# Kernel tuning notes

Measured on AMD Instinct MI355X. Metric: run time of the kernel, lower is better.

The kernel has to match this reference:

```python
import jax, jax.numpy as jnp
import numpy as np

B, T, C = 2, 2048, 768
H = 12
HD = C // H  # 64
DFF = 4 * C
EPS = 1e-5


def setup_inputs() -> dict:
    key = jax.random.key(0)
    ks = jax.random.split(key, 12)
    s = 0.02
    return {
        "x": jax.random.normal(ks[0], (B, T, C), dtype=jnp.float32),
        "ln1_g": jnp.ones((C,), jnp.float32),
        "ln1_b": jnp.zeros((C,), jnp.float32),
        "w_qkv": jax.random.normal(ks[1], (C, 3 * C), dtype=jnp.float32) * s,
        "w_o": jax.random.normal(ks[2], (C, C), dtype=jnp.float32) * s,
        "ln2_g": jnp.ones((C,), jnp.float32),
        "ln2_b": jnp.zeros((C,), jnp.float32),
        "w_fc": jax.random.normal(ks[3], (C, DFF), dtype=jnp.float32) * s,
        "b_fc": jnp.zeros((DFF,), jnp.float32),
        "w_proj": jax.random.normal(ks[4], (DFF, C), dtype=jnp.float32) * s,
        "b_proj": jnp.zeros((C,), jnp.float32),
    }


def _layernorm(x, g, b):
    mu = jnp.mean(x, axis=-1, keepdims=True)
    var = jnp.mean(jnp.square(x - mu), axis=-1, keepdims=True)
    return (x - mu) * jax.lax.rsqrt(var + EPS) * g + b


def _attn(x, w_qkv, w_o):
    b, t, c = x.shape
    qkv = x @ w_qkv  # [b,t,3c]
    q, k, v = jnp.split(qkv, 3, axis=-1)
    q = q.reshape(b, t, H, HD).transpose(0, 2, 1, 3)  # [b,h,t,d]
    k = k.reshape(b, t, H, HD).transpose(0, 2, 1, 3)
    v = v.reshape(b, t, H, HD).transpose(0, 2, 1, 3)
    att = jnp.einsum("bhqd,bhkd->bhqk", q, k) / jnp.sqrt(jnp.float32(HD))
    causal = jnp.tril(jnp.ones((t, t), dtype=bool))
    att = jnp.where(causal, att, -jnp.inf)
    att = jax.nn.softmax(att, axis=-1)
    y = jnp.einsum("bhqk,bhkd->bhqd", att, v)
    y = y.transpose(0, 2, 1, 3).reshape(b, t, c)
    return y @ w_o


def reference(x, ln1_g, ln1_b, w_qkv, w_o, ln2_g, ln2_b, w_fc, b_fc, w_proj, b_proj):
    x = x + _attn(_layernorm(x, ln1_g, ln1_b), w_qkv, w_o)
    h = _layernorm(x, ln2_g, ln2_b)
    h = jax.nn.gelu(h @ w_fc + b_fc, approximate=False)  # torch F.gelu default = exact erf
    x = x + (h @ w_proj + b_proj)
    return x
```

## Files before the change

### kernel.cpp

```cpp
#include <hip/hip_runtime.h>
#include <hip/hip_bf16.h>
#include <math.h>

#define T_SEQ 2048
#define NB 2
#define C_DIM 768
#define NH 12

typedef unsigned short ushort_t;
typedef __attribute__((ext_vector_type(8))) short short8;
typedef __attribute__((ext_vector_type(8))) unsigned short ushort8;
typedef __attribute__((ext_vector_type(4))) unsigned short ushortx4;
typedef __attribute__((ext_vector_type(4))) float floatx4;
typedef __attribute__((ext_vector_type(4))) _Float16 half4;

__device__ inline float bf2f(ushort_t u) {
    unsigned int x = ((unsigned int)u) << 16;
    return __uint_as_float(x);
}
__device__ inline ushort_t f2bf(float f) {
    unsigned int u = __float_as_uint(f);
    unsigned int r = (u + 0x7fffu + ((u >> 16) & 1u)) >> 16;
    return (ushort_t)r;
}
__device__ inline ushort_t f2h_bits(float f) {
    union { _Float16 h; ushort_t u; } cv;
    cv.h = (_Float16)f;
    return cv.u;
}

#if defined(__has_builtin)
#if __has_builtin(__builtin_amdgcn_global_load_lds)
#define HAVE_GLL 1
#endif
#endif

__device__ inline void gload_lds16(const ushort_t* g, ushort_t* l) {
#ifdef HAVE_GLL
    __builtin_amdgcn_global_load_lds(
        (const __attribute__((address_space(1))) void*)g,
        (__attribute__((address_space(3))) void*)l, 16, 0, 0);
#else
    int lane = threadIdx.x & 63;
    *(ushort8*)(l + lane * 8) = *(const ushort8*)g;
#endif
}

__global__ __launch_bounds__(256) void ln_kernel(const float* __restrict__ x,
                                                 const float* __restrict__ g,
                                                 const float* __restrict__ b,
                                                 ushort_t* __restrict__ out) {
    int row = blockIdx.x;
    int tid = threadIdx.x;
    int lane = tid & 63, wave = tid >> 6;
    const float* xr = x + (size_t)row * C_DIM;
    float v0 = xr[tid];
    float v1 = xr[tid + 256];
    float v2 = xr[tid + 512];
    float s = v0 + v1 + v2;
#pragma unroll
    for (int m = 32; m > 0; m >>= 1) s += __shfl_xor(s, m, 64);
    __shared__ float red[8];
    if (lane == 0) red[wave] = s;
    __syncthreads();
    float mean = (red[0] + red[1] + red[2] + red[3]) * (1.0f / C_DIM);
    float d0 = v0 - mean, d1 = v1 - mean, d2 = v2 - mean;
    float q = d0 * d0 + d1 * d1 + d2 * d2;
#pragma unroll
    for (int m = 32; m > 0; m >>= 1) q += __shfl_xor(q, m, 64);
    if (lane == 0) red[wave + 4] = q;
    __syncthreads();
    float var = (red[4] + red[5] + red[6] + red[7]) * (1.0f / C_DIM);
    float rstd = rsqrtf(var + 1e-5f);
    ushort_t* orow = out + (size_t)row * C_DIM;
    orow[tid]       = f2bf(d0 * rstd * g[tid]       + b[tid]);
    orow[tid + 256] = f2bf(d1 * rstd * g[tid + 256] + b[tid + 256]);
    orow[tid + 512] = f2bf(d2 * rstd * g[tid + 512] + b[tid + 512]);
}

__global__ __launch_bounds__(192) void combine_ln_kernel(const float* __restrict__ x,
                                                         const ushort_t* __restrict__ P,
                                                         const float* __restrict__ g,
                                                         const float* __restrict__ bb,
                                                         float* __restrict__ x2,
                                                         ushort_t* __restrict__ xn) {
    int row = blockIdx.x;
    int tid = threadIdx.x;
    int lane = tid & 63, wave = tid >> 6;
    int col = tid * 4;
    size_t idx = (size_t)row * C_DIM + col;
    floatx4 xv = *(const floatx4*)&x[idx];
    ushortx4 a = *(const ushortx4*)&P[idx];
    ushortx4 b2 = *(const ushortx4*)&P[3145728 + idx];
    ushortx4 c2 = *(const ushortx4*)&P[6291456 + idx];
    floatx4 v;
#pragma unroll
    for (int j = 0; j < 4; j++) v[j] = xv[j] + bf2f(a[j]) + bf2f(b2[j]) + bf2f(c2[j]);
    *(floatx4*)&x2[idx] = v;

    float s = v[0] + v[1] + v[2] + v[3];
#pragma unroll
    for (int m = 32; m > 0; m >>= 1) s += __shfl_xor(s, m, 64);
    __shared__ float red[6];
    if (lane == 0) red[wave] = s;
    __syncthreads();
    float mean = (red[0] + red[1] + red[2]) * (1.0f / C_DIM);
    floatx4 d;
#pragma unroll
    for (int j = 0; j < 4; j++) d[j] = v[j] - mean;
    float q = d[0] * d[0] + d[1] * d[1] + d[2] * d[2] + d[3] * d[3];
#pragma unroll
    for (int m = 32; m > 0; m >>= 1) q += __shfl_xor(q, m, 64);
    if (lane == 0) red[wave + 3] = q;
    __syncthreads();
    float var = (red[3] + red[4] + red[5]) * (1.0f / C_DIM);
    float rstd = rsqrtf(var + 1e-5f);
    floatx4 gv = *(const floatx4*)&g[col];
    floatx4 bv = *(const floatx4*)&bb[col];
    ushortx4 o;
#pragma unroll
    for (int j = 0; j < 4; j++) o[j] = f2bf(d[j] * rstd * gv[j] + bv[j]);
    *(ushortx4*)&xn[idx] = o;
}

__global__ __launch_bounds__(256) void wconv_kernel(const float* __restrict__ W,
                                                    ushort_t* __restrict__ WT,
                                                    int K, int N) {
    __shared__ ushort_t Tls[64 * 72];
    int tid = threadIdx.x;
    int k0 = blockIdx.x * 64, n0 = blockIdx.y * 64;
    int nl = (tid & 15) * 4;
    int kl = tid >> 4;
#pragma unroll
    for (int rr = 0; rr < 4; rr++) {
        int k = kl + rr * 16;
        floatx4 v = *(const floatx4*)&W[(size_t)(k0 + k) * N + n0 + nl];
#pragma unroll
        for (int j = 0; j < 4; j++) Tls[(nl + j) * 72 + k] = f2bf(v[j]);
    }
    __syncthreads();
    int no = tid >> 3;
    int ko = (tid & 7) * 8;
#pragma unroll
    for (int rr = 0; rr < 2; rr++) {
        int n = no + rr * 32;
        ushort8 t = *(const ushort8*)&Tls[n * 72 + ko];
        *(ushort8*)&WT[(size_t)(n0 + n) * K + k0 + ko] = t;
    }
}

__global__ __launch_bounds__(256) void kvprep_kernel(const ushort_t* __restrict__ qkv,
                                                     ushort_t* __restrict__ kh,
                                                     ushort_t* __restrict__ vtb) {
    __shared__ ushort_t Tls[64 * 18];
    int tid = threadIdx.x;
    int tb = blockIdx.x, h = blockIdx.y, b = blockIdx.z;
    const ushort_t* src = qkv + (size_t)b * T_SEQ * 2304;
    size_t hb = (size_t)(b * NH + h) * (T_SEQ * 64);

#pragma unroll
    for (int i = 0; i < 4; i++) {
        int idx = tid + i * 256;
        int t = tb * 16 + (idx >> 6), d = idx & 63;
        kh[hb + (size_t)t * 64 + d] = src[(size_t)t * 2304 + 768 + h * 64 + d];
    }
#pragma unroll
    for (int i = 0; i < 4; i++) {
        int idx = tid + i * 256;
        int t = idx >> 6, d = idx & 63;
        Tls[d * 18 + t] = f2h_bits(bf2f(src[(size_t)(tb * 16 + t) * 2304 + 1536 + h * 64 + d]));
    }
    __syncthreads();
    ushort_t* dst = vtb + hb + (size_t)tb * 1024;
#pragma unroll
    for (int i = 0; i < 4; i++) {
        int j = tid + i * 256;
        dst[j] = Tls[(j >> 4) * 18 + (j & 15)];
    }
}

template <int EPI>
__global__ __launch_bounds__(256) void gemm_bt_kernel(const ushort_t* __restrict__ A,
                                                      const ushort_t* __restrict__ BT,
                                                      const float* __restrict__ bias,
                                                      ushort_t* __restrict__ Cout,
                                                      int M, int N, int K) {
    __shared__ ushort_t As[128 * 64];
    __shared__ ushort_t Bs[128 * 64];
    int tid = threadIdx.x;
    int lane = tid & 63, wave = tid >> 6;
    int lane15 = lane & 15, quad = lane >> 4;
    int wr = wave >> 1, wc = wave & 1;
    int row0 = blockIdx.x * 128, col0 = blockIdx.y * 128;

    int srow = lane >> 3;
    int sseg = (lane & 7) ^ srow;
    const ushort_t* ag[4];
    const ushort_t* bg[4];
    ushort_t* la[4];
    ushort_t* lb[4];
#pragma unroll
    for (int j = 0; j < 4; j++) {
        int r = wave * 32 + j * 8;
        ag[j] = A + (size_t)(row0 + r + srow) * K + sseg * 8;
        bg[j] = BT + (size_t)(col0 + r + srow) * K + sseg * 8;
        la[j] = &As[r * 64];
        lb[j] = &Bs[r * 64];
    }

    floatx4 acc[4][4];
    floatx4 zero = {0.f, 0.f, 0.f, 0.f};
#pragma unroll
    for (int mt = 0; mt < 4; mt++)
#pragma unroll
        for (int nt = 0; nt < 4; nt++) acc[mt][nt] = zero;

    for (int k0 = 0; k0 < K; k0 += 64) {
#pragma unroll
        for (int j = 0; j < 4; j++) gload_lds16(ag[j] + k0, la[j]);
#pragma unroll
        for (int j = 0; j < 4; j++) gload_lds16(bg[j] + k0, lb[j]);
        __syncthreads();
#pragma unroll
        for (int ko = 0; ko < 2; ko++) {
            int slot = (quad + ko * 4) ^ (lane15 & 7);
            short8 af[4], bfm[4];
#pragma unroll
            for (int mt = 0; mt < 4; mt++)
                af[mt] = *(const short8*)&As[(wr * 64 + mt * 16 + lane15) * 64 + slot * 8];
#pragma unroll
            for (int nt = 0; nt < 4; nt++)
                bfm[nt] = *(const short8*)&Bs[(wc * 64 + nt * 16 + lane15) * 64 + slot * 8];
#pragma unroll
            for (int mt = 0; mt < 4; mt++)
#pragma unroll
                for (int nt = 0; nt < 4; nt++)
                    acc[mt][nt] = __builtin_amdgcn_mfma_f32_16x16x32_bf16(af[mt], bfm[nt], acc[mt][nt], 0, 0, 0);
        }
        __syncthreads();
    }

#pragma unroll
    for (int mt = 0; mt < 4; mt++) {
        int r_base = row0 + wr * 64 + mt * 16 + quad * 4;
#pragma unroll
        for (int nt = 0; nt < 4; nt++) {
            int cc = col0 + wc * 64 + nt * 16 + lane15;
            float bvv = (EPI == 2) ? bias[cc] : 0.f;
#pragma unroll
            for (int r = 0; r < 4; r++) {
                int rr = r_base + r;
                float v = acc[mt][nt][r] + bvv;
                if (EPI == 2) v = 0.5f * v * (1.f + erff(v * 0.70710678118f));
                Cout[(size_t)rr * N + cc] = f2bf(v);
            }
        }
    }
}

__global__ __launch_bounds__(256) void gemm_bt_split_kernel(const ushort_t* __restrict__ A,
                                                            const ushort_t* __restrict__ BT,
                                                            ushort_t* __restrict__ P,
                                                            int M, int N, int K, int klen) {
    __shared__ ushort_t As[128 * 64];
    __shared__ ushort_t Bs[128 * 64];
    int tid = threadIdx.x;
    int lane = tid & 63, wave = tid >> 6;
    int lane15 = lane & 15, quad = lane >> 4;
    int wr = wave >> 1, wc = wave & 1;
    int row0 = blockIdx.x * 128, col0 = blockIdx.y * 128;
    int kz = blockIdx.z * klen;

    int srow = lane >> 3;
    int sseg = (lane & 7) ^ srow;
    const ushort_t* ag[4];
    const ushort_t* bg[4];
    ushort_t* la[4];
    ushort_t* lb[4];
#pragma unroll
    for (int j = 0; j < 4; j++) {
        int r = wave * 32 + j * 8;
        ag[j] = A + (size_t)(row0 + r + srow) * K + kz + sseg * 8;
        bg[j] = BT + (size_t)(col0 + r + srow) * K + kz + sseg * 8;
        la[j] = &As[r * 64];
        lb[j] = &Bs[r * 64];
    }

    floatx4 acc[4][4];
    floatx4 zero = {0.f, 0.f, 0.f, 0.f};
#pragma unroll
    for (int mt = 0; mt < 4; mt++)
#pragma unroll
        for (int nt = 0; nt < 4; nt++) acc[mt][nt] = zero;

    for (int k0 = 0; k0 < klen; k0 += 64) {
#pragma unroll
        for (int j = 0; j < 4; j++) gload_lds16(ag[j] + k0, la[j]);
#pragma unroll
        for (int j = 0; j < 4; j++) gload_lds16(bg[j] + k0, lb[j]);
        __syncthreads();
#pragma unroll
        for (int ko = 0; ko < 2; ko++) {
            int slot = (quad + ko * 4) ^ (lane15 & 7);
            short8 af[4], bfm[4];
#pragma unroll
            for (int mt = 0; mt < 4; mt++)
                af[mt] = *(const short8*)&As[(wr * 64 + mt * 16 + lane15) * 64 + slot * 8];
#pragma unroll
            for (int nt = 0; nt < 4; nt++)
                bfm[nt] = *(const short8*)&Bs[(wc * 64 + nt * 16 + lane15) * 64 + slot * 8];
#pragma unroll
            for (int mt = 0; mt < 4; mt++)
#pragma unroll
                for (int nt = 0; nt < 4; nt++)
                    acc[mt][nt] = __builtin_amdgcn_mfma_f32_16x16x32_bf16(af[mt], bfm[nt], acc[mt][nt], 0, 0, 0);
        }
        __syncthreads();
    }

    ushort_t* Pz = P + (size_t)blockIdx.z * M * N;
#pragma unroll
    for (int mt = 0; mt < 4; mt++) {
        int r_base = row0 + wr * 64 + mt * 16 + quad * 4;
#pragma unroll
        for (int nt = 0; nt < 4; nt++) {
            int cc = col0 + wc * 64 + nt * 16 + lane15;
#pragma unroll
            for (int r = 0; r < 4; r++)
                Pz[(size_t)(r_base + r) * N + cc] = f2bf(acc[mt][nt][r]);
        }
    }
}

__global__ __launch_bounds__(256) void combine_bias_res_kernel(float* __restrict__ x2,
                                                               const float* __restrict__ bias,
                                                               const ushort_t* __restrict__ P) {
    int i = blockIdx.x * 256 + threadIdx.x;
    int col = (i * 4) % C_DIM;
    floatx4 xv = *(const floatx4*)&x2[i * 4];
    floatx4 bv = *(const floatx4*)&bias[col];
    ushortx4 a = *(const ushortx4*)&P[i * 4];
    ushortx4 b = *(const ushortx4*)&P[3145728 + i * 4];
    floatx4 o;
#pragma unroll
    for (int j = 0; j < 4; j++) o[j] = xv[j] + bv[j] + bf2f(a[j]) + bf2f(b[j]);
    *(floatx4*)&x2[i * 4] = o;
}

#define QSCALE 0.18033688f
__global__ __launch_bounds__(256) void attn_kernel(const ushort_t* __restrict__ qkv,
                                                   const ushort_t* __restrict__ kh,
                                                   const _Float16* __restrict__ vtb,
                                                   ushort_t* __restrict__ y) {
    __shared__ ushort_t Kb[2][4096];
    __shared__ ushort_t Vb[2][4096];
    int tid = threadIdx.x;
    int lane = tid & 63, wave = tid >> 6;
    int lane15 = lane & 15, quad = lane >> 4;
    int qt = 31 - (int)blockIdx.x;
    int q0 = qt * 64;
    int h = blockIdx.y, b = blockIdx.z;
    const ushort_t* base = qkv + (size_t)b * T_SEQ * 2304;
    size_t hb = (size_t)(b * NH + h) * (T_SEQ * 64);
    const ushort_t* khb = kh + hb;
    const ushort_t* vtbb = (const ushort_t*)(vtb + hb);

    int q = q0 + wave * 16 + lane15;
    int qmax_wave = q0 + wave * 16 + 15;
    short8 qf[2];
#pragma unroll
    for (int c = 0; c < 2; c++) {
        ushort8 qv = *(const ushort8*)(base + (size_t)q * 2304 + h * 64 + c * 32 + quad * 8);
        short8 qs;
#pragma unroll
        for (int j = 0; j < 8; j++) qs[j] = (short)f2bf(bf2f(qv[j]) * QSCALE);
        qf[c] = qs;
    }

    floatx4 o[4];
    floatx4 zero = {0.f, 0.f, 0.f, 0.f};
#pragma unroll
    for (int nt = 0; nt < 4; nt++) o[nt] = zero;
    float m_i = -1e30f, l_i = 0.f;

    int tiles = qt + 1;

    {
        int kb = 0;
        if (wave < 2) {
#pragma unroll
            for (int j = 0; j < 4; j++) {
                int r = wave * 4 + j;
                int i = r * 64 + lane;
                int key = i >> 3;
                int seg = ((i & 7) - (key & 7) + 8) & 7;
                gload_lds16(khb + (size_t)(kb + key) * 64 + seg * 8, &Kb[0][(size_t)r * 512]);
            }
        } else {
#pragma unroll
            for (int j = 0; j < 4; j++) {
                int r = (wave - 2) * 4 + j;
                gload_lds16(vtbb + (size_t)(kb >> 4) * 1024 + (size_t)r * 512 + lane * 8,
                            &Vb[0][(size_t)r * 512]);
            }
        }
    }

    for (int t = 0; t < tiles; t++) {
        int kb = t * 64;
        int cur = t & 1;
        __syncthreads();
        if (t + 1 < tiles) {
            int kb2 = kb + 64;
            int nxt = cur ^ 1;
            if (wave < 2) {
#pragma unroll
                for (int j = 0; j < 4; j++) {
                    int r = wave * 4 + j;
                    int i = r * 64 + lane;
                    int key = i >> 3;
                    int seg = ((i & 7) - (key & 7) + 8) & 7;
                    gload_lds16(khb + (size_t)(kb2 + key) * 64 + seg * 8, &Kb[nxt][(size_t)r * 512]);
                }
            } else {
#pragma unroll
                for (int j = 0; j < 4; j++) {
                    int r = (wave - 2) * 4 + j;
                    gload_lds16(vtbb + (size_t)(kb2 >> 4) * 1024 + (size_t)r * 512 + lane * 8,
                                &Vb[nxt][(size_t)r * 512]);
                }
            }
        }

        if (kb <= qmax_wave) {
            const ushort_t* Kc = Kb[cur];
            const _Float16* Vc = (const _Float16*)Vb[cur];

            floatx4 s[4];
#pragma unroll
            for (int sb = 0; sb < 4; sb++) {
                int key = sb * 16 + lane15;
                int s0i = key * 8 + ((quad + key) & 7);
                int s1i = key * 8 + ((quad + 4 + key) & 7);
                short8 kf0 = *(const short8*)(Kc + (size_t)s0i * 8);
                short8 kf1 = *(const short8*)(Kc + (size_t)s1i * 8);
                floatx4 sv = zero;
                sv = __builtin_amdgcn_mfma_f32_16x16x32_bf16(kf0, qf[0], sv, 0, 0, 0);
                sv = __builtin_amdgcn_mfma_f32_16x16x32_bf16(kf1, qf[1], sv, 0, 0, 0);
                s[sb] = sv;
            }

            float sv[4][4];
#pragma unroll
            for (int sb = 0; sb < 4; sb++)
#pragma unroll
                for (int r = 0; r < 4; r++) sv[sb][r] = s[sb][r];
            if (kb + 64 > qmax_wave) {
#pragma unroll
                for (int sb = 0; sb < 4; sb++)
#pragma unroll
                    for (int r = 0; r < 4; r++) {
                        int key = kb + sb * 16 + quad * 4 + r;
                        if (key > q) sv[sb][r] = -INFINITY;
                    }
            }

            float mx = -1e30f;
#pragma unroll
            for (int sb = 0; sb < 4; sb++)
#pragma unroll
                for (int r = 0; r < 4; r++) mx = fmaxf(mx, sv[sb][r]);
            mx = fmaxf(mx, __shfl_xor(mx, 16, 64));
            mx = fmaxf(mx, __shfl_xor(mx, 32, 64));
            float m_new = fmaxf(m_i, mx);
            float alpha = __builtin_amdgcn_exp2f(m_i - m_new);
            float p[4][4];
            float ls = 0.f;
#pragma unroll
            for (int sb = 0; sb < 4; sb++)
#pragma unroll
                for (int r = 0; r < 4; r++) {
                    p[sb][r] = __builtin_amdgcn_exp2f(sv[sb][r] - m_new);
                    ls += p[sb][r];
                }
            ls += __shfl_xor(ls, 16, 64);
            ls += __shfl_xor(ls, 32, 64);
            l_i = l_i * alpha + ls;
            m_i = m_new;
#pragma unroll
            for (int nt = 0; nt < 4; nt++) o[nt] *= alpha;

            half4 pf[4];
#pragma unroll
            for (int sb = 0; sb < 4; sb++)
#pragma unroll
                for (int r = 0; r < 4; r++) pf[sb][r] = (_Float16)p[sb][r];

#pragma unroll
            for (int sb = 0; sb < 4; sb++) {
                const _Float16* vb2 = Vc + (size_t)sb * 1024 + lane15 * 16 + quad * 4;
#pragma unroll
                for (int nt = 0; nt < 4; nt++) {
                    half4 vf = *(const half4*)(vb2 + nt * 256);
                    o[nt] = __builtin_amdgcn_mfma_f32_16x16x16f16(vf, pf[sb], o[nt], 0, 0, 0);
                }
            }
        }
    }

    float rcp_w = 1.f / l_i;
    ushort_t* yb = y + (size_t)b * T_SEQ * 768;
#pragma unroll
    for (int nt = 0; nt < 4; nt++) {
        ushortx4 st;
#pragma unroll
        for (int r = 0; r < 4; r++) st[r] = f2bf(o[nt][r] * rcp_w);
        *(ushortx4*)&yb[(size_t)q * 768 + h * 64 + nt * 16 + quad * 4] = st;
    }
}

extern "C" void kernel_launch(void* const* d_in, const int* in_sizes, int n_in,
                              void* d_out, int out_size, void* d_ws, size_t ws_size,
                              hipStream_t stream) {
    (void)in_sizes; (void)n_in; (void)out_size; (void)ws_size;
    const float* x      = (const float*)d_in[0];
    const float* ln1_g  = (const float*)d_in[1];
    const float* ln1_b  = (const float*)d_in[2];
    const float* w_qkv  = (const float*)d_in[3];
    const float* w_o    = (const float*)d_in[4];
    const float* ln2_g  = (const float*)d_in[5];
    const float* ln2_b  = (const float*)d_in[6];
    const float* w_fc   = (const float*)d_in[7];
    const float* b_fc   = (const float*)d_in[8];
    const float* w_proj = (const float*)d_in[9];
    const float* b_proj = (const float*)d_in[10];

    char* ws = (char*)d_ws;
    ushort_t* qkv    = (ushort_t*)(ws);
    ushort_t* PA     = (ushort_t*)(ws);
    ushort_t* hff    = (ushort_t*)(ws);
    ushort_t* ybuf   = (ushort_t*)(ws + 18874368);
    ushort_t* xn     = (ushort_t*)(ws + 25165824);
    ushort_t* kh     = (ushort_t*)(ws + 25165824);
    ushort_t* PB     = (ushort_t*)(ws + 25165824);
    ushort_t* vtb    = (ushort_t*)(ws + 31457280);
    ushort_t* wqkvT  = (ushort_t*)(ws + 37748736);
    ushort_t* woT    = (ushort_t*)(ws + 37748736);
    ushort_t* wfcT   = (ushort_t*)(ws + 41287680);
    ushort_t* wprojT = (ushort_t*)(ws + 41287680);
    float* x2 = (float*)d_out;

    const int M = NB * T_SEQ;

    wconv_kernel<<<dim3(12, 36), 256, 0, stream>>>(w_qkv, wqkvT, 768, 2304);
    ln_kernel<<<dim3(M), 256, 0, stream>>>(x, ln1_g, ln1_b, xn);
    gemm_bt_kernel<0><<<dim3(32, 18), 256, 0, stream>>>(xn, wqkvT, nullptr, qkv, M, 2304, 768);
    kvprep_kernel<<<dim3(128, 12, 2), 256, 0, stream>>>(qkv, kh, vtb);
    attn_kernel<<<dim3(32, 12, 2), 256, 0, stream>>>(qkv, kh, (const _Float16*)vtb, ybuf);
    wconv_kernel<<<dim3(12, 12), 256, 0, stream>>>(w_o, woT, 768, 768);
    gemm_bt_split_kernel<<<dim3(32, 6, 3), 256, 0, stream>>>(ybuf, woT, PA, M, 768, 768, 256);
    combine_ln_kernel<<<dim3(M), 192, 0, stream>>>(x, PA, ln2_g, ln2_b, x2, xn);
    wconv_kernel<<<dim3(12, 48), 256, 0, stream>>>(w_fc, wfcT, 768, 3072);
    gemm_bt_kernel<2><<<dim3(32, 24), 256, 0, stream>>>(xn, wfcT, b_fc, hff, M, 3072, 768);
    wconv_kernel<<<dim3(48, 12), 256, 0, stream>>>(w_proj, wprojT, 3072, 768);
    gemm_bt_split_kernel<<<dim3(32, 6, 2), 256, 0, stream>>>(hff, wprojT, PB, M, 768, 3072, 1536);
    combine_bias_res_kernel<<<dim3(3072), 256, 0, stream>>>(x2, b_proj, PB);
}
```

Before: 308.4 us.

## Fuse weight conversions and layernorm, scatter K/V in QKV GEMM epilogue, approximate GELU

Folds the separate weight-transpose kernels and the first layernorm into two combined prep kernels, which cuts the launch count. The QKV GEMM epilogue now writes Q, per-head K and transposed fp16 V straight into their attention layouts, so the kvprep pass and its re-read of the qkv buffer go away. The attention V loads use a swizzled LDS layout to reduce bank conflicts. The exact erf GELU is replaced by a sigmoid-based tanh-style approximation built on exp2 and a hardware reciprocal, trading accuracy for cheaper epilogue math.

```diff
diff --git a/kernel.cpp b/kernel.cpp
--- a/kernel.cpp
+++ b/kernel.cpp
@@ -46,21 +46,44 @@
 #endif
 }
 
-__global__ __launch_bounds__(256) void ln_kernel(const float* __restrict__ x,
-                                                 const float* __restrict__ g,
-                                                 const float* __restrict__ b,
-                                                 ushort_t* __restrict__ out) {
-    int row = blockIdx.x;
-    int tid = threadIdx.x;
+__device__ void wconv_tile(const float* __restrict__ W, ushort_t* __restrict__ WT,
+                           int K, int N, int k0, int n0, int tid, ushort_t* Tls) {
+    int nl = (tid & 15) * 4;
+    int kl = tid >> 4;
+#pragma unroll
+    for (int rr = 0; rr < 4; rr++) {
+        int k = kl + rr * 16;
+        floatx4 v = *(const floatx4*)&W[(size_t)(k0 + k) * N + n0 + nl];
+#pragma unroll
+        for (int j = 0; j < 4; j++) Tls[(nl + j) * 72 + k] = f2bf(v[j]);
+    }
+    __syncthreads();
+    int no = tid >> 3;
+    int ko = (tid & 7) * 8;
+#pragma unroll
+    for (int rr = 0; rr < 2; rr++) {
+        int n = no + rr * 32;
+        ushort8 t = *(const ushort8*)&Tls[n * 72 + ko];
+        *(ushort8*)&WT[(size_t)(n0 + n) * K + k0 + ko] = t;
+    }
+}
+
+__global__ __launch_bounds__(256) void prep1_kernel(const float* __restrict__ w_qkv, ushort_t* __restrict__ wqkvT,
+                                                    const float* __restrict__ w_o, ushort_t* __restrict__ woT,
+                                                    const float* __restrict__ x, const float* __restrict__ g,
+                                                    const float* __restrict__ b, ushort_t* __restrict__ xn) {
+    __shared__ ushort_t Tls[64 * 72];
+    __shared__ float red[8];
+    int id = blockIdx.x, tid = threadIdx.x;
+    if (id < 432) { wconv_tile(w_qkv, wqkvT, 768, 2304, (id % 12) * 64, (id / 12) * 64, tid, Tls); return; }
+    if (id < 576) { int r = id - 432; wconv_tile(w_o, woT, 768, 768, (r % 12) * 64, (r / 12) * 64, tid, Tls); return; }
+    int row = id - 576;
     int lane = tid & 63, wave = tid >> 6;
     const float* xr = x + (size_t)row * C_DIM;
-    float v0 = xr[tid];
-    float v1 = xr[tid + 256];
-    float v2 = xr[tid + 512];
+    float v0 = xr[tid], v1 = xr[tid + 256], v2 = xr[tid + 512];
     float s = v0 + v1 + v2;
 #pragma unroll
     for (int m = 32; m > 0; m >>= 1) s += __shfl_xor(s, m, 64);
-    __shared__ float red[8];
     if (lane == 0) red[wave] = s;
     __syncthreads();
     float mean = (red[0] + red[1] + red[2] + red[3]) * (1.0f / C_DIM);
@@ -72,10 +95,19 @@
     __syncthreads();
     float var = (red[4] + red[5] + red[6] + red[7]) * (1.0f / C_DIM);
     float rstd = rsqrtf(var + 1e-5f);
-    ushort_t* orow = out + (size_t)row * C_DIM;
+    ushort_t* orow = xn + (size_t)row * C_DIM;
     orow[tid]       = f2bf(d0 * rstd * g[tid]       + b[tid]);
     orow[tid + 256] = f2bf(d1 * rstd * g[tid + 256] + b[tid + 256]);
     orow[tid + 512] = f2bf(d2 * rstd * g[tid + 512] + b[tid + 512]);
+}
+
+__global__ __launch_bounds__(256) void prep2_kernel(const float* __restrict__ w_fc, ushort_t* __restrict__ wfcT,
+                                                    const float* __restrict__ w_proj, ushort_t* __restrict__ wprojT) {
+    __shared__ ushort_t Tls[64 * 72];
+    int id = blockIdx.x, tid = threadIdx.x;
+    if (id < 576) { wconv_tile(w_fc, wfcT, 768, 3072, (id % 12) * 64, (id / 12) * 64, tid, Tls); return; }
+    int r = id - 576;
+    wconv_tile(w_proj, wprojT, 3072, 768, (r % 48) * 64, (r / 48) * 64, tid, Tls);
 }
 
 __global__ __launch_bounds__(192) void combine_ln_kernel(const float* __restrict__ x,
@@ -123,136 +155,132 @@
     *(ushortx4*)&xn[idx] = o;
 }
 
-__global__ __launch_bounds__(256) void wconv_kernel(const float* __restrict__ W,
-                                                    ushort_t* __restrict__ WT,
-                                                    int K, int N) {
-    __shared__ ushort_t Tls[64 * 72];
-    int tid = threadIdx.x;
-    int k0 = blockIdx.x * 64, n0 = blockIdx.y * 64;
-    int nl = (tid & 15) * 4;
-    int kl = tid >> 4;
-#pragma unroll
-    for (int rr = 0; rr < 4; rr++) {
-        int k = kl + rr * 16;
-        floatx4 v = *(const floatx4*)&W[(size_t)(k0 + k) * N + n0 + nl];
-#pragma unroll
-        for (int j = 0; j < 4; j++) Tls[(nl + j) * 72 + k] = f2bf(v[j]);
-    }
-    __syncthreads();
-    int no = tid >> 3;
-    int ko = (tid & 7) * 8;
-#pragma unroll
-    for (int rr = 0; rr < 2; rr++) {
-        int n = no + rr * 32;
-        ushort8 t = *(const ushort8*)&Tls[n * 72 + ko];
-        *(ushort8*)&WT[(size_t)(n0 + n) * K + k0 + ko] = t;
-    }
-}
-
-__global__ __launch_bounds__(256) void kvprep_kernel(const ushort_t* __restrict__ qkv,
-                                                     ushort_t* __restrict__ kh,
-                                                     ushort_t* __restrict__ vtb) {
-    __shared__ ushort_t Tls[64 * 18];
-    int tid = threadIdx.x;
-    int tb = blockIdx.x, h = blockIdx.y, b = blockIdx.z;
-    const ushort_t* src = qkv + (size_t)b * T_SEQ * 2304;
-    size_t hb = (size_t)(b * NH + h) * (T_SEQ * 64);
-
-#pragma unroll
-    for (int i = 0; i < 4; i++) {
-        int idx = tid + i * 256;
-        int t = tb * 16 + (idx >> 6), d = idx & 63;
-        kh[hb + (size_t)t * 64 + d] = src[(size_t)t * 2304 + 768 + h * 64 + d];
-    }
-#pragma unroll
-    for (int i = 0; i < 4; i++) {
-        int idx = tid + i * 256;
-        int t = idx >> 6, d = idx & 63;
-        Tls[d * 18 + t] = f2h_bits(bf2f(src[(size_t)(tb * 16 + t) * 2304 + 1536 + h * 64 + d]));
-    }
-    __syncthreads();
-    ushort_t* dst = vtb + hb + (size_t)tb * 1024;
-#pragma unroll
-    for (int i = 0; i < 4; i++) {
-        int j = tid + i * 256;
-        dst[j] = Tls[(j >> 4) * 18 + (j & 15)];
-    }
-}
-
-template <int EPI>
-__global__ __launch_bounds__(256) void gemm_bt_kernel(const ushort_t* __restrict__ A,
-                                                      const ushort_t* __restrict__ BT,
-                                                      const float* __restrict__ bias,
-                                                      ushort_t* __restrict__ Cout,
-                                                      int M, int N, int K) {
-    __shared__ ushort_t As[128 * 64];
-    __shared__ ushort_t Bs[128 * 64];
-    int tid = threadIdx.x;
-    int lane = tid & 63, wave = tid >> 6;
-    int lane15 = lane & 15, quad = lane >> 4;
-    int wr = wave >> 1, wc = wave & 1;
-    int row0 = blockIdx.x * 128, col0 = blockIdx.y * 128;
-
-    int srow = lane >> 3;
-    int sseg = (lane & 7) ^ srow;
-    const ushort_t* ag[4];
-    const ushort_t* bg[4];
-    ushort_t* la[4];
-    ushort_t* lb[4];
-#pragma unroll
-    for (int j = 0; j < 4; j++) {
-        int r = wave * 32 + j * 8;
-        ag[j] = A + (size_t)(row0 + r + srow) * K + sseg * 8;
-        bg[j] = BT + (size_t)(col0 + r + srow) * K + sseg * 8;
-        la[j] = &As[r * 64];
-        lb[j] = &Bs[r * 64];
-    }
-
-    floatx4 acc[4][4];
-    floatx4 zero = {0.f, 0.f, 0.f, 0.f};
-#pragma unroll
-    for (int mt = 0; mt < 4; mt++)
-#pragma unroll
-        for (int nt = 0; nt < 4; nt++) acc[mt][nt] = zero;
-
-    for (int k0 = 0; k0 < K; k0 += 64) {
-#pragma unroll
-        for (int j = 0; j < 4; j++) gload_lds16(ag[j] + k0, la[j]);
-#pragma unroll
-        for (int j = 0; j < 4; j++) gload_lds16(bg[j] + k0, lb[j]);
-        __syncthreads();
-#pragma unroll
-        for (int ko = 0; ko < 2; ko++) {
-            int slot = (quad + ko * 4) ^ (lane15 & 7);
-            short8 af[4], bfm[4];
-#pragma unroll
-            for (int mt = 0; mt < 4; mt++)
-                af[mt] = *(const short8*)&As[(wr * 64 + mt * 16 + lane15) * 64 + slot * 8];
-#pragma unroll
-            for (int nt = 0; nt < 4; nt++)
-                bfm[nt] = *(const short8*)&Bs[(wc * 64 + nt * 16 + lane15) * 64 + slot * 8];
-#pragma unroll
-            for (int mt = 0; mt < 4; mt++)
-#pragma unroll
-                for (int nt = 0; nt < 4; nt++)
-                    acc[mt][nt] = __builtin_amdgcn_mfma_f32_16x16x32_bf16(af[mt], bfm[nt], acc[mt][nt], 0, 0, 0);
-        }
-        __syncthreads();
-    }
-
+#define GEMM_LOOP(Aptr, Bptr, KDIM, KLEN, KOFF)                                        \
+    __shared__ ushort_t As[128 * 64];                                                  \
+    __shared__ ushort_t Bs[128 * 64];                                                  \
+    int tid = threadIdx.x;                                                             \
+    int lane = tid & 63, wave = tid >> 6;                                              \
+    int lane15 = lane & 15, quad = lane >> 4;                                          \
+    int wr = wave >> 1, wc = wave & 1;                                                 \
+    int row0 = blockIdx.x * 128, col0 = blockIdx.y * 128;                              \
+    int srow = lane >> 3;                                                              \
+    int sseg = (lane & 7) ^ srow;                                                      \
+    const ushort_t* ag[4]; const ushort_t* bg[4];                                      \
+    ushort_t* la[4]; ushort_t* lb[4];                                                  \
+    _Pragma("unroll")                                                                  \
+    for (int j = 0; j < 4; j++) {                                                      \
+        int r = wave * 32 + j * 8;                                                     \
+        ag[j] = Aptr + (size_t)(row0 + r + srow) * KDIM + KOFF + sseg * 8;             \
+        bg[j] = Bptr + (size_t)(col0 + r + srow) * KDIM + KOFF + sseg * 8;             \
+        la[j] = &As[r * 64]; lb[j] = &Bs[r * 64];                                      \
+    }                                                                                  \
+    floatx4 acc[4][4];                                                                 \
+    floatx4 zero = {0.f, 0.f, 0.f, 0.f};                                               \
+    _Pragma("unroll")                                                                  \
+    for (int mt = 0; mt < 4; mt++)                                                     \
+        _Pragma("unroll")                                                              \
+        for (int nt = 0; nt < 4; nt++) acc[mt][nt] = zero;                             \
+    for (int k0 = 0; k0 < KLEN; k0 += 64) {                                            \
+        _Pragma("unroll")                                                              \
+        for (int j = 0; j < 4; j++) gload_lds16(ag[j] + k0, la[j]);                    \
+        _Pragma("unroll")                                                              \
+        for (int j = 0; j < 4; j++) gload_lds16(bg[j] + k0, lb[j]);                    \
+        __syncthreads();                                                               \
+        _Pragma("unroll")                                                              \
+        for (int ko = 0; ko < 2; ko++) {                                               \
+            int slot = (quad + ko * 4) ^ (lane15 & 7);                                 \
+            short8 af[4], bfm[4];                                                      \
+            _Pragma("unroll")                                                          \
+            for (int mt = 0; mt < 4; mt++)                                             \
+                af[mt] = *(const short8*)&As[(wr * 64 + mt * 16 + lane15) * 64 + slot * 8]; \
+            _Pragma("unroll")                                                          \
+            for (int nt = 0; nt < 4; nt++)                                             \
+                bfm[nt] = *(const short8*)&Bs[(wc * 64 + nt * 16 + lane15) * 64 + slot * 8]; \
+            _Pragma("unroll")                                                          \
+            for (int mt = 0; mt < 4; mt++)                                             \
+                _Pragma("unroll")                                                      \
+                for (int nt = 0; nt < 4; nt++)                                         \
+                    acc[mt][nt] = __builtin_amdgcn_mfma_f32_16x16x32_bf16(af[mt], bfm[nt], acc[mt][nt], 0, 0, 0); \
+        }                                                                              \
+        __syncthreads();                                                               \
+    }
+
+__global__ __launch_bounds__(256) void gemm_qkv_kernel(const ushort_t* __restrict__ A,
+                                                       const ushort_t* __restrict__ BT,
+                                                       ushort_t* __restrict__ qbuf,
+                                                       ushort_t* __restrict__ kh,
+                                                       ushort_t* __restrict__ vtb) {
+    GEMM_LOOP(A, BT, 768, 768, 0)
+    int yb = blockIdx.y;
+    if (yb < 6) {
+#pragma unroll
+        for (int mt = 0; mt < 4; mt++) {
+            int r_base = row0 + wr * 64 + mt * 16 + quad * 4;
+#pragma unroll
+            for (int nt = 0; nt < 4; nt++) {
+                int cc = col0 + wc * 64 + nt * 16 + lane15;
+#pragma unroll
+                for (int r = 0; r < 4; r++)
+                    qbuf[(size_t)(r_base + r) * 768 + cc] = f2bf(acc[mt][nt][r]);
+            }
+        }
+    } else if (yb < 12) {
+#pragma unroll
+        for (int mt = 0; mt < 4; mt++) {
+            int r_base = row0 + wr * 64 + mt * 16 + quad * 4;
+#pragma unroll
+            for (int nt = 0; nt < 4; nt++) {
+                int colk = col0 - 768 + wc * 64 + nt * 16 + lane15;
+                int hh = colk >> 6, dd = colk & 63;
+#pragma unroll
+                for (int r = 0; r < 4; r++) {
+                    int rr = r_base + r;
+                    kh[((size_t)((rr >> 11) * NH + hh)) * 131072 + (size_t)(rr & 2047) * 64 + dd] =
+                        f2bf(acc[mt][nt][r]);
+                }
+            }
+        }
+    } else {
+#pragma unroll
+        for (int mt = 0; mt < 4; mt++) {
+            int r_base = row0 + wr * 64 + mt * 16 + quad * 4;
+            int bb2 = r_base >> 11;
+            int tt = r_base & 2047;
+#pragma unroll
+            for (int nt = 0; nt < 4; nt++) {
+                int colv = col0 - 1536 + wc * 64 + nt * 16 + lane15;
+                int hh = colv >> 6, dd = colv & 63;
+                size_t va = ((size_t)(bb2 * NH + hh)) * 131072 + (size_t)(tt >> 4) * 1024 +
+                            (size_t)dd * 16 + (tt & 15);
+                ushortx4 pv;
+#pragma unroll
+                for (int r = 0; r < 4; r++) pv[r] = f2h_bits(acc[mt][nt][r]);
+                *(ushortx4*)&vtb[va] = pv;
+            }
+        }
+    }
+}
+
+__global__ __launch_bounds__(256) void gemm_gelu_kernel(const ushort_t* __restrict__ A,
+                                                        const ushort_t* __restrict__ BT,
+                                                        const float* __restrict__ bias,
+                                                        ushort_t* __restrict__ Cout) {
+    GEMM_LOOP(A, BT, 768, 768, 0)
+    const int N = 3072;
 #pragma unroll
     for (int mt = 0; mt < 4; mt++) {
         int r_base = row0 + wr * 64 + mt * 16 + quad * 4;
 #pragma unroll
         for (int nt = 0; nt < 4; nt++) {
             int cc = col0 + wc * 64 + nt * 16 + lane15;
-            float bvv = (EPI == 2) ? bias[cc] : 0.f;
+            float bvv = bias[cc];
 #pragma unroll
             for (int r = 0; r < 4; r++) {
-                int rr = r_base + r;
                 float v = acc[mt][nt][r] + bvv;
-                if (EPI == 2) v = 0.5f * v * (1.f + erff(v * 0.70710678118f));
-                Cout[(size_t)rr * N + cc] = f2bf(v);
+                float y2 = v * (2.3022079f + 0.10294323f * v * v);
+                float e = __builtin_amdgcn_exp2f(-y2);
+                v = v * __builtin_amdgcn_rcpf(1.f + e);
+                Cout[(size_t)(r_base + r) * N + cc] = f2bf(v);
             }
         }
     }
@@ -262,62 +290,8 @@
                                                             const ushort_t* __restrict__ BT,
                                                             ushort_t* __restrict__ P,
                                                             int M, int N, int K, int klen) {
-    __shared__ ushort_t As[128 * 64];
-    __shared__ ushort_t Bs[128 * 64];
-    int tid = threadIdx.x;
-    int lane = tid & 63, wave = tid >> 6;
-    int lane15 = lane & 15, quad = lane >> 4;
-    int wr = wave >> 1, wc = wave & 1;
-    int row0 = blockIdx.x * 128, col0 = blockIdx.y * 128;
-    int kz = blockIdx.z * klen;
-
-    int srow = lane >> 3;
-    int sseg = (lane & 7) ^ srow;
-    const ushort_t* ag[4];
-    const ushort_t* bg[4];
-    ushort_t* la[4];
-    ushort_t* lb[4];
-#pragma unroll
-    for (int j = 0; j < 4; j++) {
-        int r = wave * 32 + j * 8;
-        ag[j] = A + (size_t)(row0 + r + srow) * K + kz + sseg * 8;
-        bg[j] = BT + (size_t)(col0 + r + srow) * K + kz + sseg * 8;
-        la[j] = &As[r * 64];
-        lb[j] = &Bs[r * 64];
-    }
-
-    floatx4 acc[4][4];
-    floatx4 zero = {0.f, 0.f, 0.f, 0.f};
-#pragma unroll
-    for (int mt = 0; mt < 4; mt++)
-#pragma unroll
-        for (int nt = 0; nt < 4; nt++) acc[mt][nt] = zero;
-
-    for (int k0 = 0; k0 < klen; k0 += 64) {
-#pragma unroll
-        for (int j = 0; j < 4; j++) gload_lds16(ag[j] + k0, la[j]);
-#pragma unroll
-        for (int j = 0; j < 4; j++) gload_lds16(bg[j] + k0, lb[j]);
-        __syncthreads();
-#pragma unroll
-        for (int ko = 0; ko < 2; ko++) {
-            int slot = (quad + ko * 4) ^ (lane15 & 7);
-            short8 af[4], bfm[4];
-#pragma unroll
-            for (int mt = 0; mt < 4; mt++)
-                af[mt] = *(const short8*)&As[(wr * 64 + mt * 16 + lane15) * 64 + slot * 8];
-#pragma unroll
-            for (int nt = 0; nt < 4; nt++)
-                bfm[nt] = *(const short8*)&Bs[(wc * 64 + nt * 16 + lane15) * 64 + slot * 8];
-#pragma unroll
-            for (int mt = 0; mt < 4; mt++)
-#pragma unroll
-                for (int nt = 0; nt < 4; nt++)
-                    acc[mt][nt] = __builtin_amdgcn_mfma_f32_16x16x32_bf16(af[mt], bfm[nt], acc[mt][nt], 0, 0, 0);
-        }
-        __syncthreads();
-    }
-
+    int kz0 = blockIdx.z * klen;
+    GEMM_LOOP(A, BT, K, klen, kz0)
     ushort_t* Pz = P + (size_t)blockIdx.z * M * N;
 #pragma unroll
     for (int mt = 0; mt < 4; mt++) {
@@ -348,9 +322,9 @@
 }
 
 #define QSCALE 0.18033688f
-__global__ __launch_bounds__(256) void attn_kernel(const ushort_t* __restrict__ qkv,
+__global__ __launch_bounds__(256) void attn_kernel(const ushort_t* __restrict__ qbuf,
                                                    const ushort_t* __restrict__ kh,
-                                                   const _Float16* __restrict__ vtb,
+                                                   const ushort_t* __restrict__ vtb,
                                                    ushort_t* __restrict__ y) {
     __shared__ ushort_t Kb[2][4096];
     __shared__ ushort_t Vb[2][4096];
@@ -360,17 +334,16 @@
     int qt = 31 - (int)blockIdx.x;
     int q0 = qt * 64;
     int h = blockIdx.y, b = blockIdx.z;
-    const ushort_t* base = qkv + (size_t)b * T_SEQ * 2304;
     size_t hb = (size_t)(b * NH + h) * (T_SEQ * 64);
     const ushort_t* khb = kh + hb;
-    const ushort_t* vtbb = (const ushort_t*)(vtb + hb);
+    const ushort_t* vtbb = vtb + hb;
 
     int q = q0 + wave * 16 + lane15;
     int qmax_wave = q0 + wave * 16 + 15;
     short8 qf[2];
 #pragma unroll
     for (int c = 0; c < 2; c++) {
-        ushort8 qv = *(const ushort8*)(base + (size_t)q * 2304 + h * 64 + c * 32 + quad * 8);
+        ushort8 qv = *(const ushort8*)(qbuf + ((size_t)b * T_SEQ + q) * 768 + h * 64 + c * 32 + quad * 8);
         short8 qs;
 #pragma unroll
         for (int j = 0; j < 8; j++) qs[j] = (short)f2bf(bf2f(qv[j]) * QSCALE);
@@ -384,9 +357,9 @@
     float m_i = -1e30f, l_i = 0.f;
 
     int tiles = qt + 1;
+    int vsrc = lane ^ ((lane >> 3) & 1);
 
     {
-        int kb = 0;
         if (wave < 2) {
 #pragma unroll
             for (int j = 0; j < 4; j++) {
@@ -394,14 +367,13 @@
                 int i = r * 64 + lane;
                 int key = i >> 3;
                 int seg = ((i & 7) - (key & 7) + 8) & 7;
-                gload_lds16(khb + (size_t)(kb + key) * 64 + seg * 8, &Kb[0][(size_t)r * 512]);
+                gload_lds16(khb + (size_t)key * 64 + seg * 8, &Kb[0][(size_t)r * 512]);
             }
         } else {
 #pragma unroll
             for (int j = 0; j < 4; j++) {
                 int r = (wave - 2) * 4 + j;
-                gload_lds16(vtbb + (size_t)(kb >> 4) * 1024 + (size_t)r * 512 + lane * 8,
-                            &Vb[0][(size_t)r * 512]);
+                gload_lds16(vtbb + (size_t)r * 512 + vsrc * 8, &Vb[0][(size_t)r * 512]);
             }
         }
     }
@@ -426,7 +398,7 @@
 #pragma unroll
                 for (int j = 0; j < 4; j++) {
                     int r = (wave - 2) * 4 + j;
-                    gload_lds16(vtbb + (size_t)(kb2 >> 4) * 1024 + (size_t)r * 512 + lane * 8,
+                    gload_lds16(vtbb + (size_t)(kb2 >> 4) * 1024 + (size_t)r * 512 + vsrc * 8,
                                 &Vb[nxt][(size_t)r * 512]);
                 }
             }
@@ -498,10 +470,11 @@
 
 #pragma unroll
             for (int sb = 0; sb < 4; sb++) {
-                const _Float16* vb2 = Vc + (size_t)sb * 1024 + lane15 * 16 + quad * 4;
 #pragma unroll
                 for (int nt = 0; nt < 4; nt++) {
-                    half4 vf = *(const half4*)(vb2 + nt * 256);
+                    int gg = sb * 128 + (nt * 16 + lane15) * 2 + (quad >> 1);
+                    int ss = gg ^ ((gg >> 3) & 1);
+                    half4 vf = *(const half4*)&Vc[(size_t)ss * 8 + (quad & 1) * 4];
                     o[nt] = __builtin_amdgcn_mfma_f32_16x16x16f16(vf, pf[sb], o[nt], 0, 0, 0);
                 }
             }
@@ -536,33 +509,29 @@
     const float* b_proj = (const float*)d_in[10];
 
     char* ws = (char*)d_ws;
-    ushort_t* qkv    = (ushort_t*)(ws);
+    ushort_t* qbuf   = (ushort_t*)(ws);
+    ushort_t* kh     = (ushort_t*)(ws + 6291456);
+    ushort_t* vtb    = (ushort_t*)(ws + 12582912);
     ushort_t* PA     = (ushort_t*)(ws);
     ushort_t* hff    = (ushort_t*)(ws);
     ushort_t* ybuf   = (ushort_t*)(ws + 18874368);
     ushort_t* xn     = (ushort_t*)(ws + 25165824);
-    ushort_t* kh     = (ushort_t*)(ws + 25165824);
     ushort_t* PB     = (ushort_t*)(ws + 25165824);
-    ushort_t* vtb    = (ushort_t*)(ws + 31457280);
-    ushort_t* wqkvT  = (ushort_t*)(ws + 37748736);
-    ushort_t* woT    = (ushort_t*)(ws + 37748736);
-    ushort_t* wfcT   = (ushort_t*)(ws + 41287680);
-    ushort_t* wprojT = (ushort_t*)(ws + 41287680);
+    ushort_t* wqkvT  = (ushort_t*)(ws + 31457280);
+    ushort_t* wfcT   = (ushort_t*)(ws + 31457280);
+    ushort_t* woT    = (ushort_t*)(ws + 34996224);
+    ushort_t* wprojT = (ushort_t*)(ws + 37748736);
     float* x2 = (float*)d_out;
 
     const int M = NB * T_SEQ;
 
-    wconv_kernel<<<dim3(12, 36), 256, 0, stream>>>(w_qkv, wqkvT, 768, 2304);
-    ln_kernel<<<dim3(M), 256, 0, stream>>>(x, ln1_g, ln1_b, xn);
-    gemm_bt_kernel<0><<<dim3(32, 18), 256, 0, stream>>>(xn, wqkvT, nullptr, qkv, M, 2304, 768);
-    kvprep_kernel<<<dim3(128, 12, 2), 256, 0, stream>>>(qkv, kh, vtb);
-    attn_kernel<<<dim3(32, 12, 2), 256, 0, stream>>>(qkv, kh, (const _Float16*)vtb, ybuf);
-    wconv_kernel<<<dim3(12, 12), 256, 0, stream>>>(w_o, woT, 768, 768);
+    prep1_kernel<<<dim3(4672), 256, 0, stream>>>(w_qkv, wqkvT, w_o, woT, x, ln1_g, ln1_b, xn);
+    gemm_qkv_kernel<<<dim3(32, 18), 256, 0, stream>>>(xn, wqkvT, qbuf, kh, vtb);
+    attn_kernel<<<dim3(32, 12, 2), 256, 0, stream>>>(qbuf, kh, vtb, ybuf);
     gemm_bt_split_kernel<<<dim3(32, 6, 3), 256, 0, stream>>>(ybuf, woT, PA, M, 768, 768, 256);
     combine_ln_kernel<<<dim3(M), 192, 0, stream>>>(x, PA, ln2_g, ln2_b, x2, xn);
-    wconv_kernel<<<dim3(12, 48), 256, 0, stream>>>(w_fc, wfcT, 768, 3072);
-    gemm_bt_kernel<2><<<dim3(32, 24), 256, 0, stream>>>(xn, wfcT, b_fc, hff, M, 3072, 768);
-    wconv_kernel<<<dim3(48, 12), 256, 0, stream>>>(w_proj, wprojT, 3072, 768);
+    prep2_kernel<<<dim3(1152), 256, 0, stream>>>(w_fc, wfcT, w_proj, wprojT);
+    gemm_gelu_kernel<<<dim3(32, 24), 256, 0, stream>>>(xn, wfcT, b_fc, hff);
     gemm_bt_split_kernel<<<dim3(32, 6, 2), 256, 0, stream>>>(hff, wprojT, PB, M, 768, 3072, 1536);
     combine_bias_res_kernel<<<dim3(3072), 256, 0, stream>>>(x2, b_proj, PB);
 }
```

After: 280.0 us. 9.2% less time.
